# Performance work log

Hardware: AMD Instinct MI355X
Metric: run time of the kernel (lower is better)

Reference implementation:

```python
import jax, jax.numpy as jnp
import numpy as np

N, E, IN, H, ED, G, OUT = 50000, 800000, 128, 256, 32, 500, 16
LN_EPS = 1e-5
BN_EPS = 1e-5


def _w(key, shape, scale=0.05):
    return scale * jax.random.normal(key, shape, dtype=jnp.float32)


def setup_inputs() -> dict:
    key = jax.random.key(0)
    ks = iter(jax.random.split(key, 64))
    inp = {
        'x': jax.random.normal(next(ks), (N, IN), jnp.float32),
        'edge_index': jax.random.randint(next(ks), (2, E), 0, N, jnp.int64),
        'edge_attr': jax.random.normal(next(ks), (E, ED), jnp.float32),
        'batch': jnp.sort(jax.random.randint(next(ks), (N,), 0, G, jnp.int64)),
    }
    def conv_params(pfx, din):
        return {
            pfx + '_Wq': _w(next(ks), (din, H)), pfx + '_bq': jnp.zeros((H,), jnp.float32),
            pfx + '_Wk': _w(next(ks), (din, H)), pfx + '_bk': jnp.zeros((H,), jnp.float32),
            pfx + '_Wv': _w(next(ks), (din, H)), pfx + '_bv': jnp.zeros((H,), jnp.float32),
            pfx + '_We': _w(next(ks), (ED, H)),
            pfx + '_Ws': _w(next(ks), (din, H)), pfx + '_bs': jnp.zeros((H,), jnp.float32),
        }
    inp.update(conv_params('conv1', IN))
    inp.update({'ln1_g': jnp.ones((H,), jnp.float32), 'ln1_b': jnp.zeros((H,), jnp.float32)})
    inp.update(conv_params('conv2', H))
    inp.update({'ln2_g': jnp.ones((H,), jnp.float32), 'ln2_b': jnp.zeros((H,), jnp.float32)})
    for pfx in ('gin1', 'gin2'):
        inp.update({
            pfx + '_W1': _w(next(ks), (H, H)), pfx + '_b1': jnp.zeros((H,), jnp.float32),
            pfx + '_bng': jnp.ones((H,), jnp.float32), pfx + '_bnb': jnp.zeros((H,), jnp.float32),
            pfx + '_W2': _w(next(ks), (H, H)), pfx + '_b2': jnp.zeros((H,), jnp.float32),
        })
    inp.update({'lin_W': _w(next(ks), (H, H)), 'lin_b': jnp.zeros((H,), jnp.float32),
                'clf_W': _w(next(ks), (H, OUT)), 'clf_b': jnp.zeros((OUT,), jnp.float32)})
    return inp


def transformer_conv(x, src, dst, ea, Wq, bq, Wk, bk, Wv, bv, We, Ws, bs):
    # PyG TransformerConv, heads=1, edge_dim set, root_weight=True, beta=False
    h = Wq.shape[1]
    q = x @ Wq + bq                      # [N,H]
    e = ea @ We                          # [E,H]
    ke = (x @ Wk + bk)[src] + e          # [E,H]
    ve = (x @ Wv + bv)[src] + e          # [E,H]
    score = jnp.sum(q[dst] * ke, axis=-1) / jnp.sqrt(jnp.float32(h))  # [E]
    m = jax.ops.segment_max(score, dst, num_segments=N)
    ex = jnp.exp(score - m[dst])
    denom = jax.ops.segment_sum(ex, dst, num_segments=N)
    alpha = ex / (denom[dst] + 1e-16)
    out = jax.ops.segment_sum(alpha[:, None] * ve, dst, num_segments=N)
    return out + x @ Ws + bs


def layer_norm(x, g, b):
    mu = jnp.mean(x, axis=-1, keepdims=True)
    var = jnp.var(x, axis=-1, keepdims=True)
    return (x - mu) * jax.lax.rsqrt(var + LN_EPS) * g + b


def gin_conv(x, src, dst, W1, b1, bng, bnb, W2, b2):
    # GINConv(eps=0): mlp(x + sum_{j in N(i)} x_j); MLP = Linear-BN-ReLU-Linear
    agg = jax.ops.segment_sum(x[src], dst, num_segments=N)
    h = x + agg
    y = h @ W1 + b1
    mu = jnp.mean(y, axis=0)
    var = jnp.var(y, axis=0)
    y = (y - mu) * jax.lax.rsqrt(var + BN_EPS) * bng + bnb
    y = jax.nn.relu(y)
    return y @ W2 + b2


def reference(x, edge_index, edge_attr, batch,
              conv1_Wq, conv1_bq, conv1_Wk, conv1_bk, conv1_Wv, conv1_bv, conv1_We, conv1_Ws, conv1_bs,
              ln1_g, ln1_b,
              conv2_Wq, conv2_bq, conv2_Wk, conv2_bk, conv2_Wv, conv2_bv, conv2_We, conv2_Ws, conv2_bs,
              ln2_g, ln2_b,
              gin1_W1, gin1_b1, gin1_bng, gin1_bnb, gin1_W2, gin1_b2,
              gin2_W1, gin2_b1, gin2_bng, gin2_bnb, gin2_W2, gin2_b2,
              lin_W, lin_b, clf_W, clf_b):
    src, dst = edge_index[0], edge_index[1]
    # NodeEncoder (dropout inactive in eval)
    h = transformer_conv(x, src, dst, edge_attr, conv1_Wq, conv1_bq, conv1_Wk, conv1_bk,
                         conv1_Wv, conv1_bv, conv1_We, conv1_Ws, conv1_bs)
    h = layer_norm(jax.nn.leaky_relu(h), ln1_g, ln1_b)
    h = transformer_conv(h, src, dst, edge_attr, conv2_Wq, conv2_bq, conv2_Wk, conv2_bk,
                         conv2_Wv, conv2_bv, conv2_We, conv2_Ws, conv2_bs)
    h = layer_norm(jax.nn.leaky_relu(h), ln2_g, ln2_b)
    # GIN_Net, max_depth=2: conv -> relu -> conv
    h = gin_conv(h, src, dst, gin1_W1, gin1_b1, gin1_bng, gin1_bnb, gin1_W2, gin1_b2)
    h = jax.nn.relu(h)
    h = gin_conv(h, src, dst, gin2_W1, gin2_b1, gin2_bng, gin2_bnb, gin2_W2, gin2_b2)
    # global_add_pool + MLP head
    pooled = jax.ops.segment_sum(h, batch, num_segments=G)   # [G,H]
    z = jax.nn.relu(pooled @ lin_W + lin_b)
    return z @ clf_W + clf_b                                 # [G,OUT]
```

## Files before the change

### kernel.cpp

```cpp
#include <hip/hip_runtime.h>
#include <math.h>

#define NN 50000
#define NE 800000
#define DIN 128
#define DH 256
#define DED 32
#define NG 500
#define DOUT 16
#define SCAN_T 256

typedef __bf16 bf16_t;
typedef __bf16 bf16x4 __attribute__((ext_vector_type(4)));
typedef __bf16 bf16x8 __attribute__((ext_vector_type(8)));
typedef float f32x4 __attribute__((ext_vector_type(4)));

__device__ __forceinline__ void async_copy16(const bf16_t* g, bf16_t* l) {
  __builtin_amdgcn_global_load_lds(
      (const __attribute__((address_space(1))) void*)g,
      (__attribute__((address_space(3))) void*)l, 16, 0, 0);
}

__global__ void fill_i32(int* __restrict__ p, int v, int n) {
  int i = blockIdx.x * 256 + threadIdx.x;
  if (i < n) p[i] = v;
}
__global__ void cast_bf16_k(const float* __restrict__ in, bf16_t* __restrict__ o, long n) {
  long i = (long)blockIdx.x * 256 + threadIdx.x;
  if (i < n) o[i] = (bf16_t)in[i];
}

__global__ void count_k(const int* __restrict__ dst, int* __restrict__ deg) {
  int e = blockIdx.x * 256 + threadIdx.x;
  if (e < NE) atomicAdd(&deg[dst[e]], 1);
}
__global__ void scan1(const int* __restrict__ deg, int* __restrict__ rowptr,
                      int* __restrict__ bsum, int n) {
  __shared__ int s[SCAN_T];
  int t = threadIdx.x, i = blockIdx.x * SCAN_T + t;
  int v = (i < n) ? deg[i] : 0;
  s[t] = v; __syncthreads();
  for (int off = 1; off < SCAN_T; off <<= 1) {
    int add = (t >= off) ? s[t - off] : 0;
    __syncthreads(); s[t] += add; __syncthreads();
  }
  if (i < n) rowptr[i + 1] = s[t];
  if (t == SCAN_T - 1) bsum[blockIdx.x] = s[t];
}
__global__ void scan2(const int* __restrict__ bsum, int* __restrict__ boff, int nb) {
  __shared__ int s[SCAN_T];
  int t = threadIdx.x;
  int v = (t < nb) ? bsum[t] : 0;
  s[t] = v; __syncthreads();
  for (int off = 1; off < SCAN_T; off <<= 1) {
    int add = (t >= off) ? s[t - off] : 0;
    __syncthreads(); s[t] += add; __syncthreads();
  }
  boff[t] = s[t] - v;
}
__global__ void scan3(int* __restrict__ rowptr, const int* __restrict__ boff, int n) {
  int i = blockIdx.x * 256 + threadIdx.x;
  if (i < n) rowptr[i + 1] += boff[i >> 8];
  if (i == 0) rowptr[0] = 0;
}
__global__ void scatter_k(const int* __restrict__ dst, const int* __restrict__ src,
                          const int* __restrict__ rowptr, int* __restrict__ cursor,
                          int* __restrict__ esrc, int* __restrict__ eidx) {
  int e = blockIdx.x * 256 + threadIdx.x;
  if (e < NE) {
    int d = dst[e];
    int pos = rowptr[d] + atomicAdd(&cursor[d], 1);
    esrc[pos] = src[e];
    eidx[pos] = e;
  }
}
__global__ void permute_ea(const int* __restrict__ eidx, const float* __restrict__ ea,
                           bf16_t* __restrict__ eac) {
  long t = (long)blockIdx.x * 256 + threadIdx.x;
  if (t >= (long)NE * 4) return;
  int pos = (int)(t >> 2), c8 = ((int)t & 3) * 8;
  int e = eidx[pos];
  const float* sp = &ea[(size_t)e * DED + c8];
  bf16x8 o;
#pragma unroll
  for (int j = 0; j < 8; ++j) o[j] = (bf16_t)sp[j];
  *(bf16x8*)&eac[(size_t)pos * DED + c8] = o;
}

struct PackEnt { const float* src; bf16_t* dst; int K; int N; };
struct PackArgs { PackEnt e[16]; };
__global__ void pack_all(PackArgs pa) {
  PackEnt en = pa.e[blockIdx.y];
  int i = blockIdx.x * 256 + threadIdx.x;
  if (i >= en.K * en.N) return;
  int el = i & 511, f = i >> 9;
  int ntiles = en.N >> 4;
  int ks = f / ntiles, t = f - ks * ntiles;
  int lane = el >> 3, j = el & 7;
  int k = ks * 32 + (lane >> 4) * 8 + j;
  int n = t * 16 + (lane & 15);
  en.dst[i] = (bf16_t)en.src[(size_t)k * en.N + n];
}

__global__ void wqe_k(const float* __restrict__ Wq, const float* __restrict__ We,
                      const float* __restrict__ bq, float* __restrict__ Wqe,
                      float* __restrict__ bqe, int din) {
  int idx = blockIdx.x * 256 + threadIdx.x;
  if (idx < din * 32) {
    int d = idx >> 5, j = idx & 31;
    float s = 0.f;
    for (int h = 0; h < DH; ++h) s += Wq[(size_t)d * DH + h] * We[(size_t)j * DH + h];
    Wqe[idx] = s;
  }
  if (idx < 32) {
    float s = 0.f;
    for (int h = 0; h < DH; ++h) s += bq[h] * We[(size_t)idx * DH + h];
    bqe[idx] = s;
  }
}

template<int NT>
__device__ __forceinline__ void gemm_body(
    const bf16_t* __restrict__ Ab, const bf16_t* __restrict__ Wp,
    const float* __restrict__ bias, float* __restrict__ Cf, bf16_t* __restrict__ Cb,
    int M, int K, int relu, int rstride, int bx)
{
  __shared__ bf16_t Atile[4096];
  __shared__ bf16_t Btile[NT * 512];
  int tid = threadIdx.x;
  int lane = tid & 63, wv = tid >> 6;
  int base = bx * 128;
  f32x4 acc[2][NT];
#pragma unroll
  for (int rt = 0; rt < 2; ++rt)
#pragma unroll
    for (int t = 0; t < NT; ++t) acc[rt][t] = (f32x4){0.f, 0.f, 0.f, 0.f};
  int arow = wv * 32 + (lane & 15);
  int aq = (lane >> 4) * 8;
  int nk = K >> 5;
  const int NCH = 512 + NT * 64;
  for (int ks = 0; ks < nk; ++ks) {
    __syncthreads();
    for (int c = tid; c < NCH; c += 256) {
      if (c < 512) {
        int r = c >> 2, q = c & 3;
        async_copy16(Ab + (size_t)(base + r) * K + ks * 32 + q * 8, &Atile[c * 8]);
      } else {
        int cb = c - 512;
        async_copy16(Wp + (size_t)ks * NT * 512 + cb * 8, &Btile[cb * 8]);
      }
    }
    __syncthreads();
    bf16x8 a0 = *(const bf16x8*)&Atile[arow * 32 + aq];
    bf16x8 a1 = *(const bf16x8*)&Atile[(arow + 16) * 32 + aq];
#pragma unroll
    for (int t = 0; t < NT; ++t) {
      bf16x8 b = *(const bf16x8*)&Btile[t * 512 + lane * 8];
      acc[0][t] = __builtin_amdgcn_mfma_f32_16x16x32_bf16(a0, b, acc[0][t], 0, 0, 0);
      acc[1][t] = __builtin_amdgcn_mfma_f32_16x16x32_bf16(a1, b, acc[1][t], 0, 0, 0);
    }
  }
  int col_l = lane & 15;
#pragma unroll
  for (int rt = 0; rt < 2; ++rt) {
    int rbase = base + wv * 32 + rt * 16 + (lane >> 4) * 4;
#pragma unroll
    for (int t = 0; t < NT; ++t) {
      int col = t * 16 + col_l;
      float bv = bias ? bias[col] : 0.f;
#pragma unroll
      for (int r = 0; r < 4; ++r) {
        int row = rbase + r;
        if (row >= M) continue;
        float vv = acc[rt][t][r] + bv;
        if (relu) vv = fmaxf(vv, 0.f);
        if (Cf) Cf[(size_t)row * rstride + col] = vv;
        if (Cb) Cb[(size_t)row * rstride + col] = (bf16_t)vv;
      }
    }
  }
}

template<int NT>
__global__ __launch_bounds__(256, 3) void gemm_mfma(
    const bf16_t* __restrict__ Ab, const bf16_t* __restrict__ Wp,
    const float* __restrict__ bias, float* __restrict__ Cf, bf16_t* __restrict__ Cb,
    int M, int K, int relu, int rstride)
{
  gemm_body<NT>(Ab, Wp, bias, Cf, Cb, M, K, relu, rstride, blockIdx.x);
}

struct QkvsArgs { const bf16_t* w[4]; const float* bias[4]; bf16_t* outp[4]; };
__global__ __launch_bounds__(256, 3) void gemm_qkvs(
    const bf16_t* __restrict__ Ab, QkvsArgs qa, int M, int K)
{
  int which = blockIdx.y;
  gemm_body<16>(Ab, qa.w[which], qa.bias[which], nullptr, qa.outp[which], M, K, 0, 1024,
                blockIdx.x);
}

__global__ __launch_bounds__(256) void conv_edge_fused(
    const int* __restrict__ rowptr, const int* __restrict__ esrc,
    const bf16_t* __restrict__ qkvs, const bf16_t* __restrict__ eac,
    const float* __restrict__ QEf,
    bf16_t* __restrict__ AGGn, bf16_t* __restrict__ EAn)
{
  int half = threadIdx.x >> 5, l = threadIdx.x & 31;
  int n = blockIdx.x * 8 + half;
  if (n >= NN) return;
  float q[8];
  {
    bf16x8 t = *(const bf16x8*)&qkvs[(size_t)n * 1024 + l * 8];
#pragma unroll
    for (int j = 0; j < 8; ++j) q[j] = (float)t[j];
  }
  float qe[8];
#pragma unroll
  for (int j = 0; j < 8; ++j) qe[j] = 0.f;
  if (l < 4) {
    const float* p = &QEf[(size_t)n * DED + l * 8];
#pragma unroll
    for (int j = 0; j < 8; ++j) qe[j] = p[j];
  }
  float s = 0.f;
  float acc[8], eacc[8];
#pragma unroll
  for (int j = 0; j < 8; ++j) { acc[j] = 0.f; eacc[j] = 0.f; }
  int i0 = rowptr[n], i1 = rowptr[n + 1];
  int i = i0;
  for (; i + 1 < i1; i += 2) {
    int s1 = esrc[i], s2 = esrc[i + 1];
    const bf16_t* b1 = &qkvs[(size_t)s1 * 1024 + 256 + l * 8];
    const bf16_t* b2 = &qkvs[(size_t)s2 * 1024 + 256 + l * 8];
    bf16x8 k1 = *(const bf16x8*)b1;
    bf16x8 v1 = *(const bf16x8*)(b1 + 256);
    bf16x8 k2 = *(const bf16x8*)b2;
    bf16x8 v2 = *(const bf16x8*)(b2 + 256);
    float ea1[8], ea2[8];
#pragma unroll
    for (int j = 0; j < 8; ++j) { ea1[j] = 0.f; ea2[j] = 0.f; }
    if (l < 4) {
      bf16x8 t1 = *(const bf16x8*)&eac[(size_t)i * DED + l * 8];
      bf16x8 t2 = *(const bf16x8*)&eac[(size_t)(i + 1) * DED + l * 8];
#pragma unroll
      for (int j = 0; j < 8; ++j) { ea1[j] = (float)t1[j]; ea2[j] = (float)t2[j]; }
    }
    float p1 = 0.f, p2 = 0.f;
#pragma unroll
    for (int j = 0; j < 8; ++j) {
      p1 = fmaf(q[j], (float)k1[j], p1);
      p2 = fmaf(q[j], (float)k2[j], p2);
    }
#pragma unroll
    for (int j = 0; j < 8; ++j) {
      p1 = fmaf(qe[j], ea1[j], p1);
      p2 = fmaf(qe[j], ea2[j], p2);
    }
#pragma unroll
    for (int off = 16; off > 0; off >>= 1) {
      p1 += __shfl_xor(p1, off, 64);
      p2 += __shfl_xor(p2, off, 64);
    }
    float ex1 = __expf(p1 * 0.0625f);
    float ex2 = __expf(p2 * 0.0625f);
    s += ex1 + ex2;
#pragma unroll
    for (int j = 0; j < 8; ++j) {
      acc[j] = fmaf(ex1, (float)v1[j], acc[j]);
      acc[j] = fmaf(ex2, (float)v2[j], acc[j]);
    }
#pragma unroll
    for (int j = 0; j < 8; ++j) {
      eacc[j] = fmaf(ex1, ea1[j], eacc[j]);
      eacc[j] = fmaf(ex2, ea2[j], eacc[j]);
    }
  }
  if (i < i1) {
    int s1 = esrc[i];
    const bf16_t* b1 = &qkvs[(size_t)s1 * 1024 + 256 + l * 8];
    bf16x8 k1 = *(const bf16x8*)b1;
    bf16x8 v1 = *(const bf16x8*)(b1 + 256);
    float ea1[8];
#pragma unroll
    for (int j = 0; j < 8; ++j) ea1[j] = 0.f;
    if (l < 4) {
      bf16x8 t1 = *(const bf16x8*)&eac[(size_t)i * DED + l * 8];
#pragma unroll
      for (int j = 0; j < 8; ++j) ea1[j] = (float)t1[j];
    }
    float p1 = 0.f;
#pragma unroll
    for (int j = 0; j < 8; ++j) p1 = fmaf(q[j], (float)k1[j], p1);
#pragma unroll
    for (int j = 0; j < 8; ++j) p1 = fmaf(qe[j], ea1[j], p1);
#pragma unroll
    for (int off = 16; off > 0; off >>= 1) p1 += __shfl_xor(p1, off, 64);
    float ex1 = __expf(p1 * 0.0625f);
    s += ex1;
#pragma unroll
    for (int j = 0; j < 8; ++j) acc[j] = fmaf(ex1, (float)v1[j], acc[j]);
#pragma unroll
    for (int j = 0; j < 8; ++j) eacc[j] = fmaf(ex1, ea1[j], eacc[j]);
  }
  float inv = 1.f / (s + 1e-16f);
  bf16x8 o;
#pragma unroll
  for (int j = 0; j < 8; ++j) o[j] = (bf16_t)(acc[j] * inv);
  *(bf16x8*)&AGGn[(size_t)n * DH + l * 8] = o;
  if (l < 4) {
    bf16x8 eo;
#pragma unroll
    for (int j = 0; j < 8; ++j) eo[j] = (bf16_t)(eacc[j] * inv);
    *(bf16x8*)&EAn[(size_t)n * DED + l * 8] = eo;
  }
}

__global__ __launch_bounds__(256) void conv_epilogue(
    const bf16_t* __restrict__ AGGn, const bf16_t* __restrict__ E2N,
    const bf16_t* __restrict__ qkvs, const float* __restrict__ g,
    const float* __restrict__ b, bf16_t* __restrict__ out)
{
  int wv = threadIdx.x >> 6, lane = threadIdx.x & 63;
  int n = blockIdx.x * 4 + wv;
  if (n >= NN) return;
  size_t base = (size_t)n * DH + lane * 4;
  bf16x4 a = *(const bf16x4*)&AGGn[base];
  bf16x4 e2 = *(const bf16x4*)&E2N[base];
  bf16x4 sv = *(const bf16x4*)&qkvs[(size_t)n * 1024 + 768 + lane * 4];
  float v[4];
#pragma unroll
  for (int j = 0; j < 4; ++j) {
    float t = (float)a[j] + (float)e2[j] + (float)sv[j];
    v[j] = (t > 0.f) ? t : 0.01f * t;
  }
  float sum = v[0] + v[1] + v[2] + v[3];
  float sq = v[0]*v[0] + v[1]*v[1] + v[2]*v[2] + v[3]*v[3];
#pragma unroll
  for (int off = 32; off > 0; off >>= 1) {
    sum += __shfl_xor(sum, off, 64);
    sq  += __shfl_xor(sq, off, 64);
  }
  float mu = sum * (1.f / DH);
  float var = sq * (1.f / DH) - mu * mu;
  float rstd = rsqrtf(var + 1e-5f);
  bf16x4 o;
#pragma unroll
  for (int j = 0; j < 4; ++j)
    o[j] = (bf16_t)((v[j] - mu) * rstd * g[lane * 4 + j] + b[lane * 4 + j]);
  *(bf16x4*)&out[base] = o;
}

__global__ __launch_bounds__(256) void gin_gather(
    const int* __restrict__ rowptr, const int* __restrict__ esrc,
    const bf16_t* __restrict__ h, bf16_t* __restrict__ out)
{
  int half = threadIdx.x >> 5, l = threadIdx.x & 31;
  int n = blockIdx.x * 8 + half;
  if (n >= NN) return;
  size_t co = (size_t)n * DH + l * 8;
  float acc[8];
  {
    bf16x8 hv = *(const bf16x8*)&h[co];
#pragma unroll
    for (int j = 0; j < 8; ++j) acc[j] = (float)hv[j];
  }
  int i0 = rowptr[n], i1 = rowptr[n + 1];
  int i = i0;
  for (; i + 1 < i1; i += 2) {
    bf16x8 t1 = *(const bf16x8*)&h[(size_t)esrc[i] * DH + l * 8];
    bf16x8 t2 = *(const bf16x8*)&h[(size_t)esrc[i + 1] * DH + l * 8];
#pragma unroll
    for (int j = 0; j < 8; ++j) acc[j] += (float)t1[j] + (float)t2[j];
  }
  if (i < i1) {
    bf16x8 t1 = *(const bf16x8*)&h[(size_t)esrc[i] * DH + l * 8];
#pragma unroll
    for (int j = 0; j < 8; ++j) acc[j] += (float)t1[j];
  }
  bf16x8 o;
#pragma unroll
  for (int j = 0; j < 8; ++j) o[j] = (bf16_t)acc[j];
  *(bf16x8*)&out[co] = o;
}

__global__ __launch_bounds__(256) void bn_partial_na(
    const float* __restrict__ y, float* __restrict__ psum, float* __restrict__ psq)
{
  int c = threadIdx.x, b = blockIdx.x;
  float s = 0.f, ss = 0.f;
  for (int r = b; r < NN; r += 256) {
    float v = y[(size_t)r * DH + c];
    s += v; ss += v * v;
  }
  psum[b * DH + c] = s; psq[b * DH + c] = ss;
}
__global__ void bn_final_na(const float* __restrict__ psum, const float* __restrict__ psq,
                            const float* __restrict__ bng, const float* __restrict__ bnb,
                            float* __restrict__ scale, float* __restrict__ shift) {
  int c = threadIdx.x;
  float s = 0.f, ss = 0.f;
  for (int b = 0; b < 256; ++b) { s += psum[b * DH + c]; ss += psq[b * DH + c]; }
  float mu = s * (1.f / NN);
  float var = ss * (1.f / NN) - mu * mu;
  float rstd = rsqrtf(var + 1e-5f);
  float sc = bng[c] * rstd;
  scale[c] = sc;
  shift[c] = bnb[c] - mu * sc;
}
__global__ void bn_apply_relu(const float* __restrict__ y, const float* __restrict__ scale,
                              const float* __restrict__ shift, bf16_t* __restrict__ o, int n) {
  int i = blockIdx.x * 256 + threadIdx.x;
  if (i < n) {
    int c = i & (DH - 1);
    o[i] = (bf16_t)fmaxf(y[i] * scale[c] + shift[c], 0.f);
  }
}

__global__ __launch_bounds__(256) void pool_sorted(
    const int* __restrict__ batch, const float* __restrict__ h, float* __restrict__ pooled)
{
  __shared__ int s0, s1;
  int g = blockIdx.x;
  if (threadIdx.x == 0) {
    int lo = 0, hi = NN;
    while (lo < hi) { int mid = (lo + hi) >> 1; if (batch[mid] < g) lo = mid + 1; else hi = mid; }
    s0 = lo;
  }
  if (threadIdx.x == 1) {
    int lo = 0, hi = NN;
    while (lo < hi) { int mid = (lo + hi) >> 1; if (batch[mid] < g + 1) lo = mid + 1; else hi = mid; }
    s1 = lo;
  }
  __syncthreads();
  int c = threadIdx.x;
  float acc = 0.f;
  for (int r = s0; r < s1; ++r) acc += h[(size_t)r * DH + c];
  pooled[(size_t)g * DH + c] = acc;
}

__global__ __launch_bounds__(256) void gemm_bias_act(
    const float* __restrict__ A, const float* __restrict__ Wm,
    const float* __restrict__ bias, float* __restrict__ C,
    int M, int K, int Ncol, int act)
{
  __shared__ __align__(16) float As[16][68];
  __shared__ __align__(16) float Bs[16][68];
  int tid = threadIdx.x;
  int tx = tid & 15, ty = tid >> 4;
  int row0 = blockIdx.y * 64 + ty * 4;
  int col0 = blockIdx.x * 64 + tx * 4;
  float acc[4][4] = {{0.f}};
  for (int k0 = 0; k0 < K; k0 += 16) {
#pragma unroll
    for (int l = 0; l < 4; ++l) {
      int e = tid + l * 256;
      int r = e >> 4, kk = e & 15;
      int gr = blockIdx.y * 64 + r;
      As[kk][r] = (gr < M) ? A[(size_t)gr * K + k0 + kk] : 0.f;
    }
#pragma unroll
    for (int l = 0; l < 4; ++l) {
      int e = tid + l * 256;
      int kk = e >> 6, c = e & 63;
      int gc = blockIdx.x * 64 + c;
      Bs[kk][c] = (gc < Ncol) ? Wm[(size_t)(k0 + kk) * Ncol + gc] : 0.f;
    }
    __syncthreads();
#pragma unroll
    for (int kk = 0; kk < 16; ++kk) {
      float4 a4 = *(const float4*)&As[kk][ty * 4];
      float4 b4 = *(const float4*)&Bs[kk][tx * 4];
      float a[4] = {a4.x, a4.y, a4.z, a4.w};
      float b[4] = {b4.x, b4.y, b4.z, b4.w};
#pragma unroll
      for (int i = 0; i < 4; ++i)
#pragma unroll
        for (int j = 0; j < 4; ++j)
          acc[i][j] = fmaf(a[i], b[j], acc[i][j]);
    }
    __syncthreads();
  }
#pragma unroll
  for (int i = 0; i < 4; ++i) {
    int r = row0 + i;
    if (r >= M) continue;
#pragma unroll
    for (int j = 0; j < 4; ++j) {
      int c = col0 + j;
      if (c >= Ncol) continue;
      float val = acc[i][j];
      if (bias) val += bias[c];
      if (act == 1) val = fmaxf(val, 0.f);
      C[(size_t)r * Ncol + c] = val;
    }
  }
}

static inline void launch_filli(hipStream_t st, int* p, int v, long n) {
  fill_i32<<<dim3((unsigned)((n + 255) / 256)), dim3(256), 0, st>>>(p, v, (int)n);
}
static inline void launch_cast(hipStream_t st, const float* in, bf16_t* o, long n) {
  cast_bf16_k<<<dim3((unsigned)((n + 255) / 256)), dim3(256), 0, st>>>(in, o, n);
}

extern "C" void kernel_launch(void* const* d_in, const int* in_sizes, int n_in,
                              void* d_out, int out_size, void* d_ws, size_t ws_size,
                              hipStream_t stream) {
  const float* x  = (const float*)d_in[0];
  const int* ei   = (const int*)d_in[1];
  const float* ea = (const float*)d_in[2];
  const int* batch = (const int*)d_in[3];
  const int* src = ei;
  const int* dst = ei + NE;

  const float* c1[9]; for (int i = 0; i < 9; ++i) c1[i] = (const float*)d_in[4 + i];
  const float* ln1g = (const float*)d_in[13]; const float* ln1b = (const float*)d_in[14];
  const float* c2[9]; for (int i = 0; i < 9; ++i) c2[i] = (const float*)d_in[15 + i];
  const float* ln2g = (const float*)d_in[24]; const float* ln2b = (const float*)d_in[25];
  const float* g1[6]; for (int i = 0; i < 6; ++i) g1[i] = (const float*)d_in[26 + i];
  const float* g2[6]; for (int i = 0; i < 6; ++i) g2[i] = (const float*)d_in[32 + i];
  const float* linW = (const float*)d_in[38]; const float* linb = (const float*)d_in[39];
  const float* clfW = (const float*)d_in[40]; const float* clfb = (const float*)d_in[41];
  float* out = (float*)d_out;

  size_t off = 0;
  auto alloc = [&](size_t bytes) -> void* {
    void* r = (char*)d_ws + off;
    off += (bytes + 255) & ~(size_t)255;
    return r;
  };
  int* deg    = (int*)alloc(NN * 4);
  int* cursor = (int*)alloc(NN * 4);
  int* rowptr = (int*)alloc((NN + 1) * 4);
  int* esrc   = (int*)alloc((size_t)NE * 4);
  int* eidx   = (int*)alloc((size_t)NE * 4);
  int* bsum   = (int*)alloc(1024);
  int* boff   = (int*)alloc(1024);
  float* QEf   = (float*)alloc((size_t)NN * DED * 4);
  float* Yf    = (float*)alloc((size_t)NN * DH * 4);
  float* pooled = (float*)alloc((size_t)NG * DH * 4);
  float* zbuf   = (float*)alloc((size_t)NG * DH * 4);
  float* psum  = (float*)alloc(256 * DH * 4);
  float* psq   = (float*)alloc(256 * DH * 4);
  float* bnscale = (float*)alloc(DH * 4);
  float* bnshift = (float*)alloc(DH * 4);
  float* wqe_tmp1 = (float*)alloc((size_t)DIN * DED * 4);
  float* wqe_tmp2 = (float*)alloc((size_t)DH * DED * 4);
  float* bqe1 = (float*)alloc(DED * 4);
  float* bqe2 = (float*)alloc(DED * 4);
  bf16_t* qkvsb = (bf16_t*)alloc((size_t)NN * 1024 * 2);
  bf16_t* h_b = (bf16_t*)alloc((size_t)NN * DH * 2);
  bf16_t* g_b = (bf16_t*)alloc((size_t)NN * DH * 2);
  bf16_t* E2Nb = (bf16_t*)alloc((size_t)NN * DH * 2);
  bf16_t* AGGb = (bf16_t*)alloc((size_t)NN * DH * 2);
  bf16_t* EAn = (bf16_t*)alloc((size_t)NN * DED * 2);
  bf16_t* xb  = (bf16_t*)alloc((size_t)NN * DIN * 2);
  bf16_t* eac = (bf16_t*)alloc((size_t)NE * DED * 2);
  float* Hout = (float*)qkvsb;
  bf16_t* pk1q = (bf16_t*)alloc(DIN * DH * 2);
  bf16_t* pk1k = (bf16_t*)alloc(DIN * DH * 2);
  bf16_t* pk1v = (bf16_t*)alloc(DIN * DH * 2);
  bf16_t* pk1s = (bf16_t*)alloc(DIN * DH * 2);
  bf16_t* pk1qe = (bf16_t*)alloc(DIN * DED * 2);
  bf16_t* pk1we = (bf16_t*)alloc(DED * DH * 2);
  bf16_t* pk2q = (bf16_t*)alloc(DH * DH * 2);
  bf16_t* pk2k = (bf16_t*)alloc(DH * DH * 2);
  bf16_t* pk2v = (bf16_t*)alloc(DH * DH * 2);
  bf16_t* pk2s = (bf16_t*)alloc(DH * DH * 2);
  bf16_t* pk2qe = (bf16_t*)alloc(DH * DED * 2);
  bf16_t* pk2we = (bf16_t*)alloc(DED * DH * 2);
  bf16_t* pkg1a = (bf16_t*)alloc(DH * DH * 2);
  bf16_t* pkg1b = (bf16_t*)alloc(DH * DH * 2);
  bf16_t* pkg2a = (bf16_t*)alloc(DH * DH * 2);
  bf16_t* pkg2b = (bf16_t*)alloc(DH * DH * 2);
  if (ws_size < off) return;

  const int GRID_M = (NN + 127) / 128;

  launch_cast(stream, x, xb, (long)NN * DIN);
  wqe_k<<<dim3((DIN * 32 + 255) / 256), dim3(256), 0, stream>>>(c1[0], c1[6], c1[1], wqe_tmp1, bqe1, DIN);
  wqe_k<<<dim3((DH * 32 + 255) / 256), dim3(256), 0, stream>>>(c2[0], c2[6], c2[1], wqe_tmp2, bqe2, DH);
  PackArgs pa;
  pa.e[0]  = {c1[0], pk1q, DIN, DH};
  pa.e[1]  = {c1[2], pk1k, DIN, DH};
  pa.e[2]  = {c1[4], pk1v, DIN, DH};
  pa.e[3]  = {c1[7], pk1s, DIN, DH};
  pa.e[4]  = {c1[6], pk1we, DED, DH};
  pa.e[5]  = {wqe_tmp1, pk1qe, DIN, DED};
  pa.e[6]  = {c2[0], pk2q, DH, DH};
  pa.e[7]  = {c2[2], pk2k, DH, DH};
  pa.e[8]  = {c2[4], pk2v, DH, DH};
  pa.e[9]  = {c2[7], pk2s, DH, DH};
  pa.e[10] = {c2[6], pk2we, DED, DH};
  pa.e[11] = {wqe_tmp2, pk2qe, DH, DED};
  pa.e[12] = {g1[0], pkg1a, DH, DH};
  pa.e[13] = {g1[4], pkg1b, DH, DH};
  pa.e[14] = {g2[0], pkg2a, DH, DH};
  pa.e[15] = {g2[4], pkg2b, DH, DH};
  pack_all<<<dim3(256, 16), dim3(256), 0, stream>>>(pa);

  const int nb1 = (NN + SCAN_T - 1) / SCAN_T;
  launch_filli(stream, deg, 0, NN);
  launch_filli(stream, cursor, 0, NN);
  count_k<<<dim3((NE + 255) / 256), dim3(256), 0, stream>>>(dst, deg);
  scan1<<<dim3(nb1), dim3(SCAN_T), 0, stream>>>(deg, rowptr, bsum, NN);
  scan2<<<dim3(1), dim3(SCAN_T), 0, stream>>>(bsum, boff, nb1);
  scan3<<<dim3(nb1), dim3(SCAN_T), 0, stream>>>(rowptr, boff, NN);
  scatter_k<<<dim3((NE + 255) / 256), dim3(256), 0, stream>>>(dst, src, rowptr, cursor, esrc, eidx);
  permute_ea<<<dim3((unsigned)(((long)NE * 4 + 255) / 256)), dim3(256), 0, stream>>>(eidx, ea, eac);

  auto conv = [&](const bf16_t* Ain, int K,
                  const bf16_t* pq, const bf16_t* pk, const bf16_t* pv, const bf16_t* ps,
                  const bf16_t* pqe, const bf16_t* pwe,
                  const float* const* P, const float* bqe,
                  const float* lng, const float* lnb, bf16_t* outb) {
    QkvsArgs qa;
    qa.w[0] = pq; qa.w[1] = pk; qa.w[2] = pv; qa.w[3] = ps;
    qa.bias[0] = P[1]; qa.bias[1] = P[3]; qa.bias[2] = P[5]; qa.bias[3] = P[8];
    qa.outp[0] = qkvsb + 0; qa.outp[1] = qkvsb + 256;
    qa.outp[2] = qkvsb + 512; qa.outp[3] = qkvsb + 768;
    gemm_qkvs<<<dim3(GRID_M, 4), dim3(256), 0, stream>>>(Ain, qa, NN, K);
    gemm_mfma<2><<<dim3(GRID_M), dim3(256), 0, stream>>>(Ain, pqe, bqe, QEf, nullptr, NN, K, 0, 32);
    conv_edge_fused<<<dim3((NN + 7) / 8), dim3(256), 0, stream>>>(
        rowptr, esrc, qkvsb, eac, QEf, AGGb, EAn);
    gemm_mfma<16><<<dim3(GRID_M), dim3(256), 0, stream>>>(EAn, pwe, nullptr, nullptr, E2Nb, NN, DED, 0, 256);
    conv_epilogue<<<dim3((NN + 3) / 4), dim3(256), 0, stream>>>(AGGb, E2Nb, qkvsb, lng, lnb, outb);
  };

  auto gin = [&](const bf16_t* hin, const bf16_t* pw1, const bf16_t* pw2,
                 const float* const* P, int relu_out, float* Cf, bf16_t* Cb) {
    gin_gather<<<dim3((NN + 7) / 8), dim3(256), 0, stream>>>(rowptr, esrc, hin, g_b);
    gemm_mfma<16><<<dim3(GRID_M), dim3(256), 0, stream>>>(g_b, pw1, P[1], Yf, nullptr, NN, DH, 0, 256);
    bn_partial_na<<<dim3(256), dim3(256), 0, stream>>>(Yf, psum, psq);
    bn_final_na<<<dim3(1), dim3(256), 0, stream>>>(psum, psq, P[2], P[3], bnscale, bnshift);
    bn_apply_relu<<<dim3((NN * DH + 255) / 256), dim3(256), 0, stream>>>(
        Yf, bnscale, bnshift, g_b, NN * DH);
    gemm_mfma<16><<<dim3(GRID_M), dim3(256), 0, stream>>>(g_b, pw2, P[5], Cf, Cb, NN, DH, relu_out, 256);
  };

  conv(xb, DIN, pk1q, pk1k, pk1v, pk1s, pk1qe, pk1we, c1, bqe1, ln1g, ln1b, h_b);
  conv(h_b, DH, pk2q, pk2k, pk2v, pk2s, pk2qe, pk2we, c2, bqe2, ln2g, ln2b, h_b);
  gin(h_b, pkg1a, pkg1b, g1, 1, nullptr, h_b);
  gin(h_b, pkg2a, pkg2b, g2, 0, Hout, nullptr);

  pool_sorted<<<dim3(NG), dim3(256), 0, stream>>>(batch, Hout, pooled);
  gemm_bias_act<<<dim3(4, 8), dim3(256), 0, stream>>>(pooled, linW, linb, zbuf, NG, DH, DH, 1);
  gemm_bias_act<<<dim3(1, 8), dim3(256), 0, stream>>>(zbuf, clfW, clfb, out, NG, DH, DOUT, 0);
}
```

Before: 1.458 ms.

## Batch edge-index loads, fuse BN statistics into GEMM, use 64-row GEMM tiles

In the attention and GIN gather kernels, each half-wave now loads up to 32 source indices in one coalesced read and broadcasts them with shuffles. The gather loop is unrolled 4-way so more independent row loads are in flight at once. GIN batch-norm statistics are accumulated in the first GEMM's epilogue with shuffles and atomics, replacing a separate full read of Y; this relies on psum and psq being adjacent for the single zero-fill. Non-QKVS GEMMs switch to 64-row tiles to launch more blocks, and edge-attribute permutation now reads edges in order and scatters the writes.

```diff
diff --git a/kernel.cpp b/kernel.cpp
--- a/kernel.cpp
+++ b/kernel.cpp
@@ -65,21 +65,21 @@
 }
 __global__ void scatter_k(const int* __restrict__ dst, const int* __restrict__ src,
                           const int* __restrict__ rowptr, int* __restrict__ cursor,
-                          int* __restrict__ esrc, int* __restrict__ eidx) {
+                          int* __restrict__ esrc, int* __restrict__ epos) {
   int e = blockIdx.x * 256 + threadIdx.x;
   if (e < NE) {
     int d = dst[e];
     int pos = rowptr[d] + atomicAdd(&cursor[d], 1);
     esrc[pos] = src[e];
-    eidx[pos] = e;
-  }
-}
-__global__ void permute_ea(const int* __restrict__ eidx, const float* __restrict__ ea,
+    epos[e] = pos;
+  }
+}
+__global__ void permute_ea(const int* __restrict__ epos, const float* __restrict__ ea,
                            bf16_t* __restrict__ eac) {
   long t = (long)blockIdx.x * 256 + threadIdx.x;
   if (t >= (long)NE * 4) return;
-  int pos = (int)(t >> 2), c8 = ((int)t & 3) * 8;
-  int e = eidx[pos];
+  int e = (int)(t >> 2), c8 = ((int)t & 3) * 8;
+  int pos = epos[e];
   const float* sp = &ea[(size_t)e * DED + c8];
   bf16x8 o;
 #pragma unroll
@@ -119,51 +119,56 @@
   }
 }
 
-template<int NT>
+template<int NT, int RT>
 __device__ __forceinline__ void gemm_body(
     const bf16_t* __restrict__ Ab, const bf16_t* __restrict__ Wp,
     const float* __restrict__ bias, float* __restrict__ Cf, bf16_t* __restrict__ Cb,
-    int M, int K, int relu, int rstride, int bx)
+    int M, int K, int relu, int rstride, int bx,
+    float* __restrict__ psum, float* __restrict__ psq)
 {
-  __shared__ bf16_t Atile[4096];
+  __shared__ bf16_t Atile[RT * 2048];
   __shared__ bf16_t Btile[NT * 512];
   int tid = threadIdx.x;
   int lane = tid & 63, wv = tid >> 6;
-  int base = bx * 128;
-  f32x4 acc[2][NT];
-#pragma unroll
-  for (int rt = 0; rt < 2; ++rt)
+  int base = bx * (RT * 64);
+  f32x4 acc[RT][NT];
+#pragma unroll
+  for (int rt = 0; rt < RT; ++rt)
 #pragma unroll
     for (int t = 0; t < NT; ++t) acc[rt][t] = (f32x4){0.f, 0.f, 0.f, 0.f};
-  int arow = wv * 32 + (lane & 15);
+  int arow = wv * (16 * RT) + (lane & 15);
   int aq = (lane >> 4) * 8;
   int nk = K >> 5;
-  const int NCH = 512 + NT * 64;
+  const int ACH = RT * 256;
+  const int NCH = ACH + NT * 64;
   for (int ks = 0; ks < nk; ++ks) {
     __syncthreads();
     for (int c = tid; c < NCH; c += 256) {
-      if (c < 512) {
+      if (c < ACH) {
         int r = c >> 2, q = c & 3;
         async_copy16(Ab + (size_t)(base + r) * K + ks * 32 + q * 8, &Atile[c * 8]);
       } else {
-        int cb = c - 512;
+        int cb = c - ACH;
         async_copy16(Wp + (size_t)ks * NT * 512 + cb * 8, &Btile[cb * 8]);
       }
     }
     __syncthreads();
-    bf16x8 a0 = *(const bf16x8*)&Atile[arow * 32 + aq];
-    bf16x8 a1 = *(const bf16x8*)&Atile[(arow + 16) * 32 + aq];
+    bf16x8 a[RT];
+#pragma unroll
+    for (int rt = 0; rt < RT; ++rt)
+      a[rt] = *(const bf16x8*)&Atile[(arow + rt * 16) * 32 + aq];
 #pragma unroll
     for (int t = 0; t < NT; ++t) {
       bf16x8 b = *(const bf16x8*)&Btile[t * 512 + lane * 8];
-      acc[0][t] = __builtin_amdgcn_mfma_f32_16x16x32_bf16(a0, b, acc[0][t], 0, 0, 0);
-      acc[1][t] = __builtin_amdgcn_mfma_f32_16x16x32_bf16(a1, b, acc[1][t], 0, 0, 0);
+#pragma unroll
+      for (int rt = 0; rt < RT; ++rt)
+        acc[rt][t] = __builtin_amdgcn_mfma_f32_16x16x32_bf16(a[rt], b, acc[rt][t], 0, 0, 0);
     }
   }
   int col_l = lane & 15;
 #pragma unroll
-  for (int rt = 0; rt < 2; ++rt) {
-    int rbase = base + wv * 32 + rt * 16 + (lane >> 4) * 4;
+  for (int rt = 0; rt < RT; ++rt) {
+    int rbase = base + wv * (16 * RT) + rt * 16 + (lane >> 4) * 4;
 #pragma unroll
     for (int t = 0; t < NT; ++t) {
       int col = t * 16 + col_l;
@@ -179,15 +184,39 @@
       }
     }
   }
+  if (psum) {
+#pragma unroll
+    for (int t = 0; t < NT; ++t) {
+      float sc = 0.f, sq = 0.f;
+      float bv = bias[t * 16 + col_l];
+#pragma unroll
+      for (int rt = 0; rt < RT; ++rt) {
+        int rbase = base + wv * (16 * RT) + rt * 16 + (lane >> 4) * 4;
+#pragma unroll
+        for (int r = 0; r < 4; ++r) {
+          if (rbase + r >= M) continue;
+          float vv = acc[rt][t][r] + bv;
+          sc += vv; sq += vv * vv;
+        }
+      }
+      sc += __shfl_xor(sc, 16, 64); sc += __shfl_xor(sc, 32, 64);
+      sq += __shfl_xor(sq, 16, 64); sq += __shfl_xor(sq, 32, 64);
+      if (lane < 16) {
+        int col = t * 16 + lane;
+        atomicAdd(&psum[wv * DH + col], sc);
+        atomicAdd(&psq[wv * DH + col], sq);
+      }
+    }
+  }
 }
 
 template<int NT>
-__global__ __launch_bounds__(256, 3) void gemm_mfma(
+__global__ __launch_bounds__(256, 3) void gemm_r1(
     const bf16_t* __restrict__ Ab, const bf16_t* __restrict__ Wp,
     const float* __restrict__ bias, float* __restrict__ Cf, bf16_t* __restrict__ Cb,
-    int M, int K, int relu, int rstride)
+    int M, int K, int relu, int rstride, float* psum, float* psq)
 {
-  gemm_body<NT>(Ab, Wp, bias, Cf, Cb, M, K, relu, rstride, blockIdx.x);
+  gemm_body<NT, 1>(Ab, Wp, bias, Cf, Cb, M, K, relu, rstride, blockIdx.x, psum, psq);
 }
 
 struct QkvsArgs { const bf16_t* w[4]; const float* bias[4]; bf16_t* outp[4]; };
@@ -195,8 +224,8 @@
     const bf16_t* __restrict__ Ab, QkvsArgs qa, int M, int K)
 {
   int which = blockIdx.y;
-  gemm_body<16>(Ab, qa.w[which], qa.bias[which], nullptr, qa.outp[which], M, K, 0, 1024,
-                blockIdx.x);
+  gemm_body<16, 2>(Ab, qa.w[which], qa.bias[which], nullptr, qa.outp[which], M, K, 0, 1024,
+                   blockIdx.x, nullptr, nullptr);
 }
 
 __global__ __launch_bounds__(256) void conv_edge_fused(
@@ -227,80 +256,98 @@
 #pragma unroll
   for (int j = 0; j < 8; ++j) { acc[j] = 0.f; eacc[j] = 0.f; }
   int i0 = rowptr[n], i1 = rowptr[n + 1];
-  int i = i0;
-  for (; i + 1 < i1; i += 2) {
-    int s1 = esrc[i], s2 = esrc[i + 1];
-    const bf16_t* b1 = &qkvs[(size_t)s1 * 1024 + 256 + l * 8];
-    const bf16_t* b2 = &qkvs[(size_t)s2 * 1024 + 256 + l * 8];
-    bf16x8 k1 = *(const bf16x8*)b1;
-    bf16x8 v1 = *(const bf16x8*)(b1 + 256);
-    bf16x8 k2 = *(const bf16x8*)b2;
-    bf16x8 v2 = *(const bf16x8*)(b2 + 256);
-    float ea1[8], ea2[8];
-#pragma unroll
-    for (int j = 0; j < 8; ++j) { ea1[j] = 0.f; ea2[j] = 0.f; }
-    if (l < 4) {
-      bf16x8 t1 = *(const bf16x8*)&eac[(size_t)i * DED + l * 8];
-      bf16x8 t2 = *(const bf16x8*)&eac[(size_t)(i + 1) * DED + l * 8];
-#pragma unroll
-      for (int j = 0; j < 8; ++j) { ea1[j] = (float)t1[j]; ea2[j] = (float)t2[j]; }
-    }
-    float p1 = 0.f, p2 = 0.f;
-#pragma unroll
-    for (int j = 0; j < 8; ++j) {
-      p1 = fmaf(q[j], (float)k1[j], p1);
-      p2 = fmaf(q[j], (float)k2[j], p2);
-    }
-#pragma unroll
-    for (int j = 0; j < 8; ++j) {
-      p1 = fmaf(qe[j], ea1[j], p1);
-      p2 = fmaf(qe[j], ea2[j], p2);
-    }
-#pragma unroll
-    for (int off = 16; off > 0; off >>= 1) {
-      p1 += __shfl_xor(p1, off, 64);
-      p2 += __shfl_xor(p2, off, 64);
-    }
-    float ex1 = __expf(p1 * 0.0625f);
-    float ex2 = __expf(p2 * 0.0625f);
-    s += ex1 + ex2;
-#pragma unroll
-    for (int j = 0; j < 8; ++j) {
-      acc[j] = fmaf(ex1, (float)v1[j], acc[j]);
-      acc[j] = fmaf(ex2, (float)v2[j], acc[j]);
-    }
-#pragma unroll
-    for (int j = 0; j < 8; ++j) {
-      eacc[j] = fmaf(ex1, ea1[j], eacc[j]);
-      eacc[j] = fmaf(ex2, ea2[j], eacc[j]);
-    }
-  }
-  if (i < i1) {
-    int s1 = esrc[i];
-    const bf16_t* b1 = &qkvs[(size_t)s1 * 1024 + 256 + l * 8];
-    bf16x8 k1 = *(const bf16x8*)b1;
-    bf16x8 v1 = *(const bf16x8*)(b1 + 256);
-    float ea1[8];
-#pragma unroll
-    for (int j = 0; j < 8; ++j) ea1[j] = 0.f;
-    if (l < 4) {
-      bf16x8 t1 = *(const bf16x8*)&eac[(size_t)i * DED + l * 8];
-#pragma unroll
-      for (int j = 0; j < 8; ++j) ea1[j] = (float)t1[j];
-    }
-    float p1 = 0.f;
-#pragma unroll
-    for (int j = 0; j < 8; ++j) p1 = fmaf(q[j], (float)k1[j], p1);
-#pragma unroll
-    for (int j = 0; j < 8; ++j) p1 = fmaf(qe[j], ea1[j], p1);
-#pragma unroll
-    for (int off = 16; off > 0; off >>= 1) p1 += __shfl_xor(p1, off, 64);
-    float ex1 = __expf(p1 * 0.0625f);
-    s += ex1;
-#pragma unroll
-    for (int j = 0; j < 8; ++j) acc[j] = fmaf(ex1, (float)v1[j], acc[j]);
-#pragma unroll
-    for (int j = 0; j < 8; ++j) eacc[j] = fmaf(ex1, ea1[j], eacc[j]);
+  for (int wb = i0; wb < i1; wb += 32) {
+    int wcnt = min(32, i1 - wb);
+    int widx = (l < wcnt) ? esrc[wb + l] : 0;
+    int e = 0;
+    for (; e + 4 <= wcnt; e += 4) {
+      int s1 = __shfl(widx, e, 32);
+      int s2 = __shfl(widx, e + 1, 32);
+      int s3 = __shfl(widx, e + 2, 32);
+      int s4 = __shfl(widx, e + 3, 32);
+      const bf16_t* b1 = &qkvs[(size_t)s1 * 1024 + 256 + l * 8];
+      const bf16_t* b2 = &qkvs[(size_t)s2 * 1024 + 256 + l * 8];
+      const bf16_t* b3 = &qkvs[(size_t)s3 * 1024 + 256 + l * 8];
+      const bf16_t* b4 = &qkvs[(size_t)s4 * 1024 + 256 + l * 8];
+      bf16x8 k1 = *(const bf16x8*)b1;
+      bf16x8 k2 = *(const bf16x8*)b2;
+      bf16x8 k3 = *(const bf16x8*)b3;
+      bf16x8 k4 = *(const bf16x8*)b4;
+      bf16x8 v1 = *(const bf16x8*)(b1 + 256);
+      bf16x8 v2 = *(const bf16x8*)(b2 + 256);
+      bf16x8 v3 = *(const bf16x8*)(b3 + 256);
+      bf16x8 v4 = *(const bf16x8*)(b4 + 256);
+      bf16x8 t1 = {}, t2 = {}, t3 = {}, t4 = {};
+      if (l < 4) {
+        const bf16_t* ep = &eac[(size_t)(wb + e) * DED + l * 8];
+        t1 = *(const bf16x8*)ep;
+        t2 = *(const bf16x8*)(ep + DED);
+        t3 = *(const bf16x8*)(ep + 2 * DED);
+        t4 = *(const bf16x8*)(ep + 3 * DED);
+      }
+      float p1 = 0.f, p2 = 0.f, p3 = 0.f, p4 = 0.f;
+#pragma unroll
+      for (int j = 0; j < 8; ++j) {
+        p1 = fmaf(q[j], (float)k1[j], p1);
+        p2 = fmaf(q[j], (float)k2[j], p2);
+        p3 = fmaf(q[j], (float)k3[j], p3);
+        p4 = fmaf(q[j], (float)k4[j], p4);
+      }
+#pragma unroll
+      for (int j = 0; j < 8; ++j) {
+        p1 = fmaf(qe[j], (float)t1[j], p1);
+        p2 = fmaf(qe[j], (float)t2[j], p2);
+        p3 = fmaf(qe[j], (float)t3[j], p3);
+        p4 = fmaf(qe[j], (float)t4[j], p4);
+      }
+#pragma unroll
+      for (int off = 16; off > 0; off >>= 1) {
+        p1 += __shfl_xor(p1, off, 64);
+        p2 += __shfl_xor(p2, off, 64);
+        p3 += __shfl_xor(p3, off, 64);
+        p4 += __shfl_xor(p4, off, 64);
+      }
+      float ex1 = __expf(p1 * 0.0625f);
+      float ex2 = __expf(p2 * 0.0625f);
+      float ex3 = __expf(p3 * 0.0625f);
+      float ex4 = __expf(p4 * 0.0625f);
+      s += (ex1 + ex2) + (ex3 + ex4);
+#pragma unroll
+      for (int j = 0; j < 8; ++j) {
+        acc[j] = fmaf(ex1, (float)v1[j], acc[j]);
+        acc[j] = fmaf(ex2, (float)v2[j], acc[j]);
+        acc[j] = fmaf(ex3, (float)v3[j], acc[j]);
+        acc[j] = fmaf(ex4, (float)v4[j], acc[j]);
+      }
+#pragma unroll
+      for (int j = 0; j < 8; ++j) {
+        eacc[j] = fmaf(ex1, (float)t1[j], eacc[j]);
+        eacc[j] = fmaf(ex2, (float)t2[j], eacc[j]);
+        eacc[j] = fmaf(ex3, (float)t3[j], eacc[j]);
+        eacc[j] = fmaf(ex4, (float)t4[j], eacc[j]);
+      }
+    }
+    for (; e < wcnt; ++e) {
+      int s1 = __shfl(widx, e, 32);
+      const bf16_t* b1 = &qkvs[(size_t)s1 * 1024 + 256 + l * 8];
+      bf16x8 k1 = *(const bf16x8*)b1;
+      bf16x8 v1 = *(const bf16x8*)(b1 + 256);
+      bf16x8 t1 = {};
+      if (l < 4) t1 = *(const bf16x8*)&eac[(size_t)(wb + e) * DED + l * 8];
+      float p1 = 0.f;
+#pragma unroll
+      for (int j = 0; j < 8; ++j) p1 = fmaf(q[j], (float)k1[j], p1);
+#pragma unroll
+      for (int j = 0; j < 8; ++j) p1 = fmaf(qe[j], (float)t1[j], p1);
+#pragma unroll
+      for (int off = 16; off > 0; off >>= 1) p1 += __shfl_xor(p1, off, 64);
+      float ex1 = __expf(p1 * 0.0625f);
+      s += ex1;
+#pragma unroll
+      for (int j = 0; j < 8; ++j) acc[j] = fmaf(ex1, (float)v1[j], acc[j]);
+#pragma unroll
+      for (int j = 0; j < 8; ++j) eacc[j] = fmaf(ex1, (float)t1[j], eacc[j]);
+    }
   }
   float inv = 1.f / (s + 1e-16f);
   bf16x8 o;
@@ -365,17 +412,29 @@
     for (int j = 0; j < 8; ++j) acc[j] = (float)hv[j];
   }
   int i0 = rowptr[n], i1 = rowptr[n + 1];
-  int i = i0;
-  for (; i + 1 < i1; i += 2) {
-    bf16x8 t1 = *(const bf16x8*)&h[(size_t)esrc[i] * DH + l * 8];
-    bf16x8 t2 = *(const bf16x8*)&h[(size_t)esrc[i + 1] * DH + l * 8];
-#pragma unroll
-    for (int j = 0; j < 8; ++j) acc[j] += (float)t1[j] + (float)t2[j];
-  }
-  if (i < i1) {
-    bf16x8 t1 = *(const bf16x8*)&h[(size_t)esrc[i] * DH + l * 8];
-#pragma unroll
-    for (int j = 0; j < 8; ++j) acc[j] += (float)t1[j];
+  for (int wb = i0; wb < i1; wb += 32) {
+    int wcnt = min(32, i1 - wb);
+    int widx = (l < wcnt) ? esrc[wb + l] : 0;
+    int e = 0;
+    for (; e + 4 <= wcnt; e += 4) {
+      int s1 = __shfl(widx, e, 32);
+      int s2 = __shfl(widx, e + 1, 32);
+      int s3 = __shfl(widx, e + 2, 32);
+      int s4 = __shfl(widx, e + 3, 32);
+      bf16x8 t1 = *(const bf16x8*)&h[(size_t)s1 * DH + l * 8];
+      bf16x8 t2 = *(const bf16x8*)&h[(size_t)s2 * DH + l * 8];
+      bf16x8 t3 = *(const bf16x8*)&h[(size_t)s3 * DH + l * 8];
+      bf16x8 t4 = *(const bf16x8*)&h[(size_t)s4 * DH + l * 8];
+#pragma unroll
+      for (int j = 0; j < 8; ++j)
+        acc[j] += ((float)t1[j] + (float)t2[j]) + ((float)t3[j] + (float)t4[j]);
+    }
+    for (; e < wcnt; ++e) {
+      int s1 = __shfl(widx, e, 32);
+      bf16x8 t1 = *(const bf16x8*)&h[(size_t)s1 * DH + l * 8];
+#pragma unroll
+      for (int j = 0; j < 8; ++j) acc[j] += (float)t1[j];
+    }
   }
   bf16x8 o;
 #pragma unroll
@@ -383,23 +442,12 @@
   *(bf16x8*)&out[co] = o;
 }
 
-__global__ __launch_bounds__(256) void bn_partial_na(
-    const float* __restrict__ y, float* __restrict__ psum, float* __restrict__ psq)
-{
-  int c = threadIdx.x, b = blockIdx.x;
-  float s = 0.f, ss = 0.f;
-  for (int r = b; r < NN; r += 256) {
-    float v = y[(size_t)r * DH + c];
-    s += v; ss += v * v;
-  }
-  psum[b * DH + c] = s; psq[b * DH + c] = ss;
-}
 __global__ void bn_final_na(const float* __restrict__ psum, const float* __restrict__ psq,
                             const float* __restrict__ bng, const float* __restrict__ bnb,
                             float* __restrict__ scale, float* __restrict__ shift) {
   int c = threadIdx.x;
   float s = 0.f, ss = 0.f;
-  for (int b = 0; b < 256; ++b) { s += psum[b * DH + c]; ss += psq[b * DH + c]; }
+  for (int b = 0; b < 4; ++b) { s += psum[b * DH + c]; ss += psq[b * DH + c]; }
   float mu = s * (1.f / NN);
   float var = ss * (1.f / NN) - mu * mu;
   float rstd = rsqrtf(var + 1e-5f);
@@ -533,15 +581,15 @@
   int* cursor = (int*)alloc(NN * 4);
   int* rowptr = (int*)alloc((NN + 1) * 4);
   int* esrc   = (int*)alloc((size_t)NE * 4);
-  int* eidx   = (int*)alloc((size_t)NE * 4);
+  int* epos   = (int*)alloc((size_t)NE * 4);
   int* bsum   = (int*)alloc(1024);
   int* boff   = (int*)alloc(1024);
   float* QEf   = (float*)alloc((size_t)NN * DED * 4);
   float* Yf    = (float*)alloc((size_t)NN * DH * 4);
   float* pooled = (float*)alloc((size_t)NG * DH * 4);
   float* zbuf   = (float*)alloc((size_t)NG * DH * 4);
-  float* psum  = (float*)alloc(256 * DH * 4);
-  float* psq   = (float*)alloc(256 * DH * 4);
+  float* psum  = (float*)alloc(4 * DH * 4);
+  float* psq   = (float*)alloc(4 * DH * 4);
   float* bnscale = (float*)alloc(DH * 4);
   float* bnshift = (float*)alloc(DH * 4);
   float* wqe_tmp1 = (float*)alloc((size_t)DIN * DED * 4);
@@ -575,7 +623,8 @@
   bf16_t* pkg2b = (bf16_t*)alloc(DH * DH * 2);
   if (ws_size < off) return;
 
-  const int GRID_M = (NN + 127) / 128;
+  const int GRID_M  = (NN + 127) / 128;
+  const int GRID_M1 = (NN + 63) / 64;
 
   launch_cast(stream, x, xb, (long)NN * DIN);
   wqe_k<<<dim3((DIN * 32 + 255) / 256), dim3(256), 0, stream>>>(c1[0], c1[6], c1[1], wqe_tmp1, bqe1, DIN);
@@ -606,8 +655,8 @@
   scan1<<<dim3(nb1), dim3(SCAN_T), 0, stream>>>(deg, rowptr, bsum, NN);
   scan2<<<dim3(1), dim3(SCAN_T), 0, stream>>>(bsum, boff, nb1);
   scan3<<<dim3(nb1), dim3(SCAN_T), 0, stream>>>(rowptr, boff, NN);
-  scatter_k<<<dim3((NE + 255) / 256), dim3(256), 0, stream>>>(dst, src, rowptr, cursor, esrc, eidx);
-  permute_ea<<<dim3((unsigned)(((long)NE * 4 + 255) / 256)), dim3(256), 0, stream>>>(eidx, ea, eac);
+  scatter_k<<<dim3((NE + 255) / 256), dim3(256), 0, stream>>>(dst, src, rowptr, cursor, esrc, epos);
+  permute_ea<<<dim3((unsigned)(((long)NE * 4 + 255) / 256)), dim3(256), 0, stream>>>(epos, ea, eac);
 
   auto conv = [&](const bf16_t* Ain, int K,
                   const bf16_t* pq, const bf16_t* pk, const bf16_t* pv, const bf16_t* ps,
@@ -620,22 +669,26 @@
     qa.outp[0] = qkvsb + 0; qa.outp[1] = qkvsb + 256;
     qa.outp[2] = qkvsb + 512; qa.outp[3] = qkvsb + 768;
     gemm_qkvs<<<dim3(GRID_M, 4), dim3(256), 0, stream>>>(Ain, qa, NN, K);
-    gemm_mfma<2><<<dim3(GRID_M), dim3(256), 0, stream>>>(Ain, pqe, bqe, QEf, nullptr, NN, K, 0, 32);
+    gemm_r1<2><<<dim3(GRID_M1), dim3(256), 0, stream>>>(
+        Ain, pqe, bqe, QEf, nullptr, NN, K, 0, 32, nullptr, nullptr);
     conv_edge_fused<<<dim3((NN + 7) / 8), dim3(256), 0, stream>>>(
         rowptr, esrc, qkvsb, eac, QEf, AGGb, EAn);
-    gemm_mfma<16><<<dim3(GRID_M), dim3(256), 0, stream>>>(EAn, pwe, nullptr, nullptr, E2Nb, NN, DED, 0, 256);
+    gemm_r1<16><<<dim3(GRID_M1), dim3(256), 0, stream>>>(
+        EAn, pwe, nullptr, nullptr, E2Nb, NN, DED, 0, 256, nullptr, nullptr);
     conv_epilogue<<<dim3((NN + 3) / 4), dim3(256), 0, stream>>>(AGGb, E2Nb, qkvsb, lng, lnb, outb);
   };
 
   auto gin = [&](const bf16_t* hin, const bf16_t* pw1, const bf16_t* pw2,
                  const float* const* P, int relu_out, float* Cf, bf16_t* Cb) {
     gin_gather<<<dim3((NN + 7) / 8), dim3(256), 0, stream>>>(rowptr, esrc, hin, g_b);
-    gemm_mfma<16><<<dim3(GRID_M), dim3(256), 0, stream>>>(g_b, pw1, P[1], Yf, nullptr, NN, DH, 0, 256);
-    bn_partial_na<<<dim3(256), dim3(256), 0, stream>>>(Yf, psum, psq);
+    launch_filli(stream, (int*)psum, 0, 2 * 4 * DH);
+    gemm_r1<16><<<dim3(GRID_M1), dim3(256), 0, stream>>>(
+        g_b, pw1, P[1], Yf, nullptr, NN, DH, 0, 256, psum, psq);
     bn_final_na<<<dim3(1), dim3(256), 0, stream>>>(psum, psq, P[2], P[3], bnscale, bnshift);
     bn_apply_relu<<<dim3((NN * DH + 255) / 256), dim3(256), 0, stream>>>(
         Yf, bnscale, bnshift, g_b, NN * DH);
-    gemm_mfma<16><<<dim3(GRID_M), dim3(256), 0, stream>>>(g_b, pw2, P[5], Cf, Cb, NN, DH, relu_out, 256);
+    gemm_r1<16><<<dim3(GRID_M1), dim3(256), 0, stream>>>(
+        g_b, pw2, P[5], Cf, Cb, NN, DH, relu_out, 256, nullptr, nullptr);
   };
 
   conv(xb, DIN, pk1q, pk1k, pk1v, pk1s, pk1qe, pk1we, c1, bqe1, ln1g, ln1b, h_b);
```

After: 1.358 ms. -6.9%, faster.
